# Optimization experiments

Hardware: AMD Instinct MI355X
Metric: run time of the kernel (lower is better)

## Reference

```python
import jax, jax.numpy as jnp
import numpy as np

B, N0, D0, N1, D1 = 128, 64, 32, 64, 32
K = 65  # depthwise conv kernel size
SCALE = 5.0
FOCUS = 3.0
EPS_Z = float(jnp.finfo(jnp.float32).eps)


def setup_inputs() -> dict:
    key = jax.random.key(0)
    k1, k2, k3, kw, kc, kb = jax.random.split(key, 6)
    x1 = jax.random.normal(k1, (B, N0, D0), dtype=jnp.float32)
    x2 = jax.random.normal(k2, (B, N0, D0), dtype=jnp.float32)
    x3 = jax.random.normal(k3, (B, N0, D0), dtype=jnp.float32)
    # kaiming_normal_ on W [N1, N0, D0, D1]: fan_in = N0*D0*D1 per torch default on 4D
    fan_in = N0 * D0 * D1
    W = jax.random.normal(kw, (N1, N0, D0, D1), dtype=jnp.float32) * np.sqrt(2.0 / fan_in)
    # Conv1d(N1*D1, N1*D1, K, groups=N1): weight [out_ch, in_ch/groups, K]
    cin_g = D1
    bound = 1.0 / np.sqrt(cin_g * K)
    conv_w = jax.random.uniform(kc, (N1 * D1, cin_g, K), dtype=jnp.float32, minval=-bound, maxval=bound)
    conv_b = jax.random.uniform(kb, (N1 * D1,), dtype=jnp.float32, minval=-bound, maxval=bound)
    return {"x1": x1, "x2": x2, "x3": x3, "W": W, "conv_w": conv_w, "conv_b": conv_b}


def _transform(x, W):
    # x: [B, N0, D0], W: [N1, N0, D0, D1] -> u: [B, N1*D1, N0]
    u = jnp.einsum('bji,kjiz->bkjz', x, W)        # [B, N1, N0, D1]
    u = jnp.transpose(u, (0, 1, 3, 2))             # [B, N1, D1, N0]
    return u.reshape(u.shape[0], N1 * D1, N0)


def _focus(u):
    # ReLU kernel + focusing-factor renormalization along last dim
    u = jax.nn.relu(u) + 1e-6
    u = u / SCALE
    n = jnp.linalg.norm(u, axis=-1, keepdims=True)
    up = u ** FOCUS
    return up / jnp.linalg.norm(up, axis=-1, keepdims=True) * n


def _squash(x, eps=1e-20):
    norm = jnp.linalg.norm(x, axis=-1, keepdims=True)
    coef = 1.0 - 1.0 / (jnp.exp(norm) + eps)
    return coef * (x / (norm + eps))


def reference(x1, x2, x3, W, conv_w, conv_b):
    u1 = _focus(_transform(x1, W))  # [B, N1*D1, N0]
    u2 = _focus(_transform(x2, W))
    u3 = _focus(_transform(x3, W))
    z = 1.0 / (jnp.einsum('bic,bc->bi', u1, u1.sum(axis=1)) + EPS_Z)  # [B, N1*D1]
    kv = jnp.einsum('bjc,bjd->bcd', u2, u3)                           # [B, N0, N0]
    x = jnp.einsum('bic,bcd,bi->bid', u1, kv, z)                      # [B, N1*D1, N0]
    # grouped (depthwise-per-capsule) conv1d, 'same' padding
    y = jax.lax.conv_general_dilated(
        x, conv_w, window_strides=(1,), padding=[(K // 2, K // 2)],
        dimension_numbers=('NCH', 'OIH', 'NCH'), feature_group_count=N1)
    y = y + conv_b[None, :, None]
    out = (x + y).sum(axis=-1).reshape(-1, N1, D1)  # [B, N1, D1]
    return _squash(out)
```

## Files before the change

kernel.cpp:

```cpp
#include <hip/hip_runtime.h>
#include <cstddef>

#define NB 128
#define NT 64
#define ND 32
#define NG 64
#define NC 2048
#define KW 65
#define EPSZ 1.1920928955078125e-07f

#define OFF_URAW 0ull
#define SZ_URAW  (3ull * NB * NT * NC)
#define OFF_F    (OFF_URAW + SZ_URAW)
#define SZ_F     (3ull * NB * NC)
#define OFF_S1   (OFF_F + SZ_F)
#define SZ_S1    ((unsigned long long)NB * NT)
#define OFF_KV   (OFF_S1 + SZ_S1)
#define SZ_KV    ((unsigned long long)NB * NT * NT)

__global__ __launch_bounds__(256) void k_transform(
    const float* __restrict__ x1, const float* __restrict__ x2,
    const float* __restrict__ x3, const float* __restrict__ W,
    float* __restrict__ uraw) {
  int bid = blockIdx.x;
  int j   = bid & 63;
  int nt  = (bid >> 6) & 15;
  int inp = bid >> 10;
  const float* x = (inp == 0) ? x1 : ((inp == 1) ? x2 : x3);
  float* uout = uraw + (size_t)inp * ((size_t)NB * NT * NC);

  __shared__ float as[32][132];
  __shared__ float bs[32][132];
  int tid = threadIdx.x;

  {
    int b = tid >> 1, h = tid & 1;
    const float* xp = x + ((size_t)b * NT + j) * ND + h * 16;
#pragma unroll
    for (int q = 0; q < 4; ++q) {
      float4 v = *reinterpret_cast<const float4*>(xp + q * 4);
      int i0 = h * 16 + q * 4;
      as[i0 + 0][b] = v.x; as[i0 + 1][b] = v.y;
      as[i0 + 2][b] = v.z; as[i0 + 3][b] = v.w;
    }
  }
  {
    int kk = tid >> 6, u = tid & 63;
    int i = u >> 1, h = u & 1;
    const float* wp = W + (((size_t)(nt * 4 + kk) * NT + j) * ND + i) * ND + h * 16;
#pragma unroll
    for (int q = 0; q < 4; ++q) {
      float4 v = *reinterpret_cast<const float4*>(wp + q * 4);
      int c0 = kk * 32 + h * 16 + q * 4;
      bs[i][c0 + 0] = v.x; bs[i][c0 + 1] = v.y;
      bs[i][c0 + 2] = v.z; bs[i][c0 + 3] = v.w;
    }
  }
  __syncthreads();

  int tm = tid & 15, tn = tid >> 4;
  int m0 = tm * 8, n0 = tn * 8;
  float acc[8][8];
#pragma unroll
  for (int a = 0; a < 8; ++a)
#pragma unroll
    for (int c = 0; c < 8; ++c) acc[a][c] = 0.f;

#pragma unroll 4
  for (int kk = 0; kk < 32; ++kk) {
    float4 a0 = *reinterpret_cast<const float4*>(&as[kk][m0]);
    float4 a1 = *reinterpret_cast<const float4*>(&as[kk][m0 + 4]);
    float4 b0 = *reinterpret_cast<const float4*>(&bs[kk][n0]);
    float4 b1 = *reinterpret_cast<const float4*>(&bs[kk][n0 + 4]);
    float av[8] = {a0.x, a0.y, a0.z, a0.w, a1.x, a1.y, a1.z, a1.w};
    float bv[8] = {b0.x, b0.y, b0.z, b0.w, b1.x, b1.y, b1.z, b1.w};
#pragma unroll
    for (int mi = 0; mi < 8; ++mi)
#pragma unroll
      for (int ni = 0; ni < 8; ++ni)
        acc[mi][ni] = fmaf(av[mi], bv[ni], acc[mi][ni]);
  }

#pragma unroll
  for (int mi = 0; mi < 8; ++mi) {
    float* cp = uout + ((size_t)(m0 + mi) * NT + j) * NC + nt * 128 + n0;
    float4 v0 = {acc[mi][0], acc[mi][1], acc[mi][2], acc[mi][3]};
    float4 v1 = {acc[mi][4], acc[mi][5], acc[mi][6], acc[mi][7]};
    *reinterpret_cast<float4*>(cp)     = v0;
    *reinterpret_cast<float4*>(cp + 4) = v1;
  }
}

__global__ __launch_bounds__(256) void k_factors(
    const float* __restrict__ uraw, float* __restrict__ f) {
  int bid = blockIdx.x;
  const float* u = uraw + (size_t)bid * ((size_t)NT * NC);
  int tid = threadIdx.x;
  float s2[8], s6[8];
#pragma unroll
  for (int q = 0; q < 8; ++q) { s2[q] = 0.f; s6[q] = 0.f; }
  for (int t = 0; t < NT; ++t) {
    const float* row = u + (size_t)t * NC;
#pragma unroll
    for (int q = 0; q < 8; ++q) {
      float v = row[tid + q * 256];
      float up = (fmaxf(v, 0.f) + 1e-6f) * 0.2f;
      float p2 = up * up;
      float p3 = p2 * up;
      s2[q] += p2;
      s6[q] += p3 * p3;
    }
  }
#pragma unroll
  for (int q = 0; q < 8; ++q)
    f[(size_t)bid * NC + tid + q * 256] = sqrtf(s2[q]) / sqrtf(s6[q]);
}

__global__ void k_zero(float* __restrict__ p, int n) {
  int i = blockIdx.x * blockDim.x + threadIdx.x;
  int stride = gridDim.x * blockDim.x;
  for (; i < n; i += stride) p[i] = 0.f;
}

__global__ __launch_bounds__(256) void k_kv_s1(
    const float* __restrict__ uraw, const float* __restrict__ f,
    float* __restrict__ kv, float* __restrict__ s1) {
  int b = blockIdx.x >> 2, chq = blockIdx.x & 3;
  int chbase = chq * 512;
  const float* u1 = uraw + (size_t)b * ((size_t)NT * NC);
  const float* u2 = u1 + (size_t)NB * NT * NC;
  const float* u3 = u2 + (size_t)NB * NT * NC;
  const float* f1 = f + (size_t)b * NC;
  const float* f2 = f1 + (size_t)NB * NC;
  const float* f3 = f2 + (size_t)NB * NC;

  __shared__ float a2[64][68];
  __shared__ float a3[64][68];
  __shared__ float red[64][4];
  int tid = threadIdx.x;

  {
    int t = tid >> 2, cq = tid & 3;
    const float* up = u1 + (size_t)t * NC + chbase + cq * 128;
    const float* fp = f1 + chbase + cq * 128;
    float acc = 0.f;
#pragma unroll 4
    for (int q = 0; q < 32; ++q) {
      float4 v  = *reinterpret_cast<const float4*>(up + q * 4);
      float4 fv = *reinterpret_cast<const float4*>(fp + q * 4);
      float vv[4] = {v.x, v.y, v.z, v.w};
      float ff[4] = {fv.x, fv.y, fv.z, fv.w};
#pragma unroll
      for (int r = 0; r < 4; ++r) {
        float uu = (fmaxf(vv[r], 0.f) + 1e-6f) * 0.2f;
        acc += uu * uu * uu * ff[r];
      }
    }
    red[t][cq] = acc;
  }
  __syncthreads();
  if (tid < 64)
    atomicAdd(&s1[b * NT + tid],
              red[tid][0] + red[tid][1] + red[tid][2] + red[tid][3]);

  int tm = tid & 15, tn = tid >> 4;
  float acc[4][4];
#pragma unroll
  for (int r = 0; r < 4; ++r)
#pragma unroll
    for (int q = 0; q < 4; ++q) acc[r][q] = 0.f;

  for (int tile = 0; tile < 8; ++tile) {
    int ch0 = chbase + tile * 64;
    __syncthreads();
    {
      int t = tid >> 2, c4 = tid & 3;
#pragma unroll
      for (int q = 0; q < 4; ++q) {
        int c = c4 * 16 + q * 4;
        float4 v2 = *reinterpret_cast<const float4*>(u2 + (size_t)t * NC + ch0 + c);
        float4 g2 = *reinterpret_cast<const float4*>(f2 + ch0 + c);
        float4 v3 = *reinterpret_cast<const float4*>(u3 + (size_t)t * NC + ch0 + c);
        float4 g3 = *reinterpret_cast<const float4*>(f3 + ch0 + c);
        float vv2[4] = {v2.x, v2.y, v2.z, v2.w};
        float gg2[4] = {g2.x, g2.y, g2.z, g2.w};
        float vv3[4] = {v3.x, v3.y, v3.z, v3.w};
        float gg3[4] = {g3.x, g3.y, g3.z, g3.w};
#pragma unroll
        for (int r = 0; r < 4; ++r) {
          float uu = (fmaxf(vv2[r], 0.f) + 1e-6f) * 0.2f;
          a2[c + r][t] = uu * uu * uu * gg2[r];
          float ww = (fmaxf(vv3[r], 0.f) + 1e-6f) * 0.2f;
          a3[c + r][t] = ww * ww * ww * gg3[r];
        }
      }
    }
    __syncthreads();
#pragma unroll 8
    for (int ch = 0; ch < 64; ++ch) {
      float4 av = *reinterpret_cast<const float4*>(&a2[ch][tm * 4]);
      float4 bv = *reinterpret_cast<const float4*>(&a3[ch][tn * 4]);
      float aa[4] = {av.x, av.y, av.z, av.w};
      float bb[4] = {bv.x, bv.y, bv.z, bv.w};
#pragma unroll
      for (int r = 0; r < 4; ++r)
#pragma unroll
        for (int q = 0; q < 4; ++q)
          acc[r][q] = fmaf(aa[r], bb[q], acc[r][q]);
    }
  }
#pragma unroll
  for (int r = 0; r < 4; ++r)
#pragma unroll
    for (int q = 0; q < 4; ++q)
      atomicAdd(&kv[(size_t)b * (NT * NT) + (tm * 4 + r) * NT + tn * 4 + q],
                acc[r][q]);
}

__global__ __launch_bounds__(64) void k_cwt(
    const float* __restrict__ cw, float* __restrict__ cwt) {
  int o = blockIdx.x;
  int tid = threadIdx.x;
  __shared__ float row[32 * KW];
  for (int i = tid; i < 32 * KW; i += 64) row[i] = cw[(size_t)o * (32 * KW) + i];
  __syncthreads();
  int jj = tid, j = jj + 1;
  for (int ci = 0; ci < 32; ++ci) {
    float v = 0.f;
    if (j <= 32) v -= row[ci * KW + j + 32];
    if (j >= 32 && j <= 63) v += row[ci * KW + j - 32];
    if (j == 64) {
      float s = 0.f;
      for (int k = 32; k <= 64; ++k) s += row[ci * KW + k];
      v += s;
    }
    cwt[(size_t)o * 2048 + ci * 64 + jj] = v;
  }
}

__global__ __launch_bounds__(256) void k_pre(
    const float* __restrict__ uraw, const float* __restrict__ f,
    const float* __restrict__ kvg, const float* __restrict__ s1g,
    float* __restrict__ pre) {
  int b = blockIdx.x >> 2, q = blockIdx.x & 3;
  int chbase = q * 512;
  const float* u1 = uraw + (size_t)b * ((size_t)NT * NC);
  const float* f1 = f + (size_t)b * NC;
  int tid = threadIdx.x;

  __shared__ float kvpreL[64][68];
  __shared__ float s1L[64];
  __shared__ float utL[64][132];

#pragma unroll
  for (int qq = 0; qq < 16; ++qq) {
    int i = tid + qq * 256;
    kvpreL[i >> 6][i & 63] = kvg[(size_t)b * (NT * NT) + i];
  }
  if (tid < 64) s1L[tid] = s1g[b * NT + tid];
  __syncthreads();
  if (tid < 64) {
    float run = 0.f;
    for (int t2 = 0; t2 < 64; ++t2) {
      run += kvpreL[tid][t2];
      kvpreL[tid][t2] = run;
    }
  }

  int cg = tid >> 3, tg = tid & 7;
  for (int tile = 0; tile < 4; ++tile) {
    int ch0 = chbase + tile * 128;
    __syncthreads();
    {
      int t = tid >> 2, c4 = tid & 3;
      const float* up = u1 + (size_t)t * NC + ch0 + c4 * 32;
      const float* fp = f1 + ch0 + c4 * 32;
#pragma unroll
      for (int qq = 0; qq < 8; ++qq) {
        float4 v  = *reinterpret_cast<const float4*>(up + qq * 4);
        float4 fv = *reinterpret_cast<const float4*>(fp + qq * 4);
        float vv[4] = {v.x, v.y, v.z, v.w};
        float ff[4] = {fv.x, fv.y, fv.z, fv.w};
#pragma unroll
        for (int r = 0; r < 4; ++r) {
          float uu = (fmaxf(vv[r], 0.f) + 1e-6f) * 0.2f;
          utL[t][c4 * 33 + qq * 4 + r] = uu * uu * uu * ff[r];
        }
      }
    }
    __syncthreads();

    int cl = cg * 4;
    int sk = (cl >> 5) * 33 + (cl & 31);
    float acc[4][8];
#pragma unroll
    for (int r = 0; r < 4; ++r)
#pragma unroll
      for (int c = 0; c < 8; ++c) acc[r][c] = 0.f;
    float accz[4] = {0.f, 0.f, 0.f, 0.f};

#pragma unroll 4
    for (int t1 = 0; t1 < 64; ++t1) {
      float4 a = *reinterpret_cast<const float4*>(&utL[t1][sk]);
      float s = s1L[t1];
      float4 k0 = *reinterpret_cast<const float4*>(&kvpreL[t1][tg * 8]);
      float4 k1 = *reinterpret_cast<const float4*>(&kvpreL[t1][tg * 8 + 4]);
      float aa[4] = {a.x, a.y, a.z, a.w};
      float kk[8] = {k0.x, k0.y, k0.z, k0.w, k1.x, k1.y, k1.z, k1.w};
#pragma unroll
      for (int r = 0; r < 4; ++r) {
        accz[r] = fmaf(aa[r], s, accz[r]);
#pragma unroll
        for (int c = 0; c < 8; ++c)
          acc[r][c] = fmaf(aa[r], kk[c], acc[r][c]);
      }
    }
#pragma unroll
    for (int r = 0; r < 4; ++r) {
      float z = 1.f / (accz[r] + EPSZ);
      float* pp = pre + ((size_t)b * NC + ch0 + cl + r) * 64 + tg * 8;
      float4 o0 = {acc[r][0] * z, acc[r][1] * z, acc[r][2] * z, acc[r][3] * z};
      float4 o1 = {acc[r][4] * z, acc[r][5] * z, acc[r][6] * z, acc[r][7] * z};
      *reinterpret_cast<float4*>(pp)     = o0;
      *reinterpret_cast<float4*>(pp + 4) = o1;
    }
  }
}

__global__ __launch_bounds__(256) void k_gemm(
    const float* __restrict__ pre, const float* __restrict__ cwt,
    const float* __restrict__ cb, float* __restrict__ out) {
  int g = blockIdx.x >> 2, bq = blockIdx.x & 3;
  int b0 = bq * 32;
  int tid = threadIdx.x;
  int oh = tid & 15, bh = tid >> 4;

  __shared__ float preL[32][68];
  __shared__ float cwtL[32][68];

  float a00 = 0.f, a01 = 0.f, a10 = 0.f, a11 = 0.f;
  float xs00 = 0.f, xs01 = 0.f, xs10 = 0.f, xs11 = 0.f;

  for (int kc = 0; kc < 32; ++kc) {
    __syncthreads();
    {
      int r8 = tid >> 3, s8 = tid & 7;
      const float* ps = pre + ((size_t)(b0 + r8) * NC + g * 32) * 64 + kc * 64 + s8 * 8;
      float4 p0 = *reinterpret_cast<const float4*>(ps);
      float4 p1 = *reinterpret_cast<const float4*>(ps + 4);
      *reinterpret_cast<float4*>(&preL[r8][s8 * 8])     = p0;
      *reinterpret_cast<float4*>(&preL[r8][s8 * 8 + 4]) = p1;
      const float* cs = cwt + (size_t)(g * 32 + r8) * 2048 + kc * 64 + s8 * 8;
      float4 c0 = *reinterpret_cast<const float4*>(cs);
      float4 c1 = *reinterpret_cast<const float4*>(cs + 4);
      *reinterpret_cast<float4*>(&cwtL[r8][s8 * 8])     = c0;
      *reinterpret_cast<float4*>(&cwtL[r8][s8 * 8 + 4]) = c1;
    }
    __syncthreads();

    if (kc == oh)      { xs00 = preL[bh][63]; xs10 = preL[bh + 16][63]; }
    if (kc == oh + 16) { xs01 = preL[bh][63]; xs11 = preL[bh + 16][63]; }

#pragma unroll
    for (int kk = 0; kk < 64; kk += 4) {
      float4 p0 = *reinterpret_cast<const float4*>(&preL[bh][kk]);
      float4 p1 = *reinterpret_cast<const float4*>(&preL[bh + 16][kk]);
      float4 c0 = *reinterpret_cast<const float4*>(&cwtL[oh][kk]);
      float4 c1 = *reinterpret_cast<const float4*>(&cwtL[oh + 16][kk]);
      a00 = fmaf(p0.x, c0.x, a00); a00 = fmaf(p0.y, c0.y, a00);
      a00 = fmaf(p0.z, c0.z, a00); a00 = fmaf(p0.w, c0.w, a00);
      a01 = fmaf(p0.x, c1.x, a01); a01 = fmaf(p0.y, c1.y, a01);
      a01 = fmaf(p0.z, c1.z, a01); a01 = fmaf(p0.w, c1.w, a01);
      a10 = fmaf(p1.x, c0.x, a10); a10 = fmaf(p1.y, c0.y, a10);
      a10 = fmaf(p1.z, c0.z, a10); a10 = fmaf(p1.w, c0.w, a10);
      a11 = fmaf(p1.x, c1.x, a11); a11 = fmaf(p1.y, c1.y, a11);
      a11 = fmaf(p1.z, c1.z, a11); a11 = fmaf(p1.w, c1.w, a11);
    }
  }

  float cb0 = cb[g * 32 + oh], cb1 = cb[g * 32 + oh + 16];
  float v00 = a00 + xs00 + 64.f * cb0;
  float v01 = a01 + xs01 + 64.f * cb1;
  float v10 = a10 + xs10 + 64.f * cb0;
  float v11 = a11 + xs11 + 64.f * cb1;

  float sqA = v00 * v00 + v01 * v01;
  float sqB = v10 * v10 + v11 * v11;
#pragma unroll
  for (int m = 8; m >= 1; m >>= 1) {
    sqA += __shfl_xor(sqA, m, 16);
    sqB += __shfl_xor(sqB, m, 16);
  }
  float nA = sqrtf(sqA), nB = sqrtf(sqB);
  float cA = 1.f - 1.f / (expf(nA) + 1e-20f);
  float cB = 1.f - 1.f / (expf(nB) + 1e-20f);
  float iA = cA / (nA + 1e-20f), iB = cB / (nB + 1e-20f);

  size_t baseA = ((size_t)(b0 + bh) * NG + g) * ND;
  size_t baseB = ((size_t)(b0 + bh + 16) * NG + g) * ND;
  out[baseA + oh]      = v00 * iA;
  out[baseA + oh + 16] = v01 * iA;
  out[baseB + oh]      = v10 * iB;
  out[baseB + oh + 16] = v11 * iB;
}

extern "C" void kernel_launch(void* const* d_in, const int* in_sizes, int n_in,
                              void* d_out, int out_size, void* d_ws, size_t ws_size,
                              hipStream_t stream) {
  const float* x1 = (const float*)d_in[0];
  const float* x2 = (const float*)d_in[1];
  const float* x3 = (const float*)d_in[2];
  const float* W  = (const float*)d_in[3];
  const float* cw = (const float*)d_in[4];
  const float* cb = (const float*)d_in[5];
  float* out = (float*)d_out;

  float* ws   = (float*)d_ws;
  float* uraw = ws + OFF_URAW;
  float* f    = ws + OFF_F;
  float* s1   = ws + OFF_S1;
  float* kv   = ws + OFF_KV;
  float* pre  = uraw + (size_t)NB * NT * NC;
  float* cwt  = uraw + 2ull * NB * NT * NC;

  k_transform<<<3072, 256, 0, stream>>>(x1, x2, x3, W, uraw);
  k_factors<<<384, 256, 0, stream>>>(uraw, f);
  k_zero<<<512, 256, 0, stream>>>(s1, (int)(SZ_S1 + SZ_KV));
  k_kv_s1<<<512, 256, 0, stream>>>(uraw, f, kv, s1);
  k_cwt<<<2048, 64, 0, stream>>>(cw, cwt);
  k_pre<<<512, 256, 0, stream>>>(uraw, f, kv, s1, pre);
  k_gemm<<<256, 256, 0, stream>>>(pre, cwt, cb, out);
}
```

Before: 361.6 us.

## Raise grid parallelism across factor, kv, pre and conv-GEMM kernels with split-K atomics

Splits k_factors into 1536 blocks, each covering a 512-channel quarter of one batch and input, and moves the s1 reduction into k_factors using wave shuffles and atomics. k_kv and k_pre now use 8 channel chunks per batch instead of 4. The final conv GEMM is rewritten as a split-K kernel that accumulates into a zeroed ysum buffer with atomics, followed by a separate k_out kernel that applies the squash. The goal is to fill more CUs on the small grids, at the cost of extra launches, extra atomics and u1 being read twice in k_factors.

```diff
diff --git a/kernel.cpp b/kernel.cpp
--- a/kernel.cpp
+++ b/kernel.cpp
@@ -92,28 +92,46 @@
 }
 
 __global__ __launch_bounds__(256) void k_factors(
-    const float* __restrict__ uraw, float* __restrict__ f) {
+    const float* __restrict__ uraw, float* __restrict__ f,
+    float* __restrict__ s1) {
   int bid = blockIdx.x;
-  const float* u = uraw + (size_t)bid * ((size_t)NT * NC);
-  int tid = threadIdx.x;
-  float s2[8], s6[8];
-#pragma unroll
-  for (int q = 0; q < 8; ++q) { s2[q] = 0.f; s6[q] = 0.f; }
+  int q = bid & 3, b = (bid >> 2) & 127, inp = bid >> 9;
+  const float* u = uraw + ((size_t)inp * NB + b) * ((size_t)NT * NC);
+  int tid = threadIdx.x;
+  int ch = q * 512 + tid * 2;
+
+  float s2a = 0.f, s6a = 0.f, s2b = 0.f, s6b = 0.f;
   for (int t = 0; t < NT; ++t) {
-    const float* row = u + (size_t)t * NC;
-#pragma unroll
-    for (int q = 0; q < 8; ++q) {
-      float v = row[tid + q * 256];
-      float up = (fmaxf(v, 0.f) + 1e-6f) * 0.2f;
-      float p2 = up * up;
-      float p3 = p2 * up;
-      s2[q] += p2;
-      s6[q] += p3 * p3;
-    }
-  }
-#pragma unroll
-  for (int q = 0; q < 8; ++q)
-    f[(size_t)bid * NC + tid + q * 256] = sqrtf(s2[q]) / sqrtf(s6[q]);
+    float2 v = *reinterpret_cast<const float2*>(u + (size_t)t * NC + ch);
+    float ua = (fmaxf(v.x, 0.f) + 1e-6f) * 0.2f;
+    float p2a = ua * ua, p3a = p2a * ua;
+    s2a += p2a; s6a += p3a * p3a;
+    float ub = (fmaxf(v.y, 0.f) + 1e-6f) * 0.2f;
+    float p2b = ub * ub, p3b = p2b * ub;
+    s2b += p2b; s6b += p3b * p3b;
+  }
+  float fa = sqrtf(s2a) / sqrtf(s6a);
+  float fb = sqrtf(s2b) / sqrtf(s6b);
+  float2 fv = {fa, fb};
+  *reinterpret_cast<float2*>(f + ((size_t)inp * NB + b) * NC + ch) = fv;
+
+  if (inp == 0) {
+    __shared__ float part[NT][4];
+    int wid = tid >> 6, lane = tid & 63;
+    for (int t = 0; t < NT; ++t) {
+      float2 v = *reinterpret_cast<const float2*>(u + (size_t)t * NC + ch);
+      float ua = (fmaxf(v.x, 0.f) + 1e-6f) * 0.2f;
+      float ub = (fmaxf(v.y, 0.f) + 1e-6f) * 0.2f;
+      float val = ua * ua * ua * fa + ub * ub * ub * fb;
+#pragma unroll
+      for (int m = 32; m >= 1; m >>= 1) val += __shfl_xor(val, m, 64);
+      if (lane == 0) part[t][wid] = val;
+    }
+    __syncthreads();
+    if (tid < NT)
+      atomicAdd(&s1[b * NT + tid],
+                part[tid][0] + part[tid][1] + part[tid][2] + part[tid][3]);
+  }
 }
 
 __global__ void k_zero(float* __restrict__ p, int n) {
@@ -122,46 +140,19 @@
   for (; i < n; i += stride) p[i] = 0.f;
 }
 
-__global__ __launch_bounds__(256) void k_kv_s1(
+__global__ __launch_bounds__(256) void k_kv(
     const float* __restrict__ uraw, const float* __restrict__ f,
-    float* __restrict__ kv, float* __restrict__ s1) {
-  int b = blockIdx.x >> 2, chq = blockIdx.x & 3;
-  int chbase = chq * 512;
-  const float* u1 = uraw + (size_t)b * ((size_t)NT * NC);
-  const float* u2 = u1 + (size_t)NB * NT * NC;
-  const float* u3 = u2 + (size_t)NB * NT * NC;
-  const float* f1 = f + (size_t)b * NC;
-  const float* f2 = f1 + (size_t)NB * NC;
-  const float* f3 = f2 + (size_t)NB * NC;
+    float* __restrict__ kv) {
+  int b = blockIdx.x >> 3, chq = blockIdx.x & 7;
+  int chbase = chq * 256;
+  const float* u2 = uraw + ((size_t)NB + b) * ((size_t)NT * NC);
+  const float* u3 = uraw + (2ull * NB + b) * ((size_t)NT * NC);
+  const float* f2 = f + ((size_t)NB + b) * NC;
+  const float* f3 = f + (2ull * NB + b) * NC;
 
   __shared__ float a2[64][68];
   __shared__ float a3[64][68];
-  __shared__ float red[64][4];
-  int tid = threadIdx.x;
-
-  {
-    int t = tid >> 2, cq = tid & 3;
-    const float* up = u1 + (size_t)t * NC + chbase + cq * 128;
-    const float* fp = f1 + chbase + cq * 128;
-    float acc = 0.f;
-#pragma unroll 4
-    for (int q = 0; q < 32; ++q) {
-      float4 v  = *reinterpret_cast<const float4*>(up + q * 4);
-      float4 fv = *reinterpret_cast<const float4*>(fp + q * 4);
-      float vv[4] = {v.x, v.y, v.z, v.w};
-      float ff[4] = {fv.x, fv.y, fv.z, fv.w};
-#pragma unroll
-      for (int r = 0; r < 4; ++r) {
-        float uu = (fmaxf(vv[r], 0.f) + 1e-6f) * 0.2f;
-        acc += uu * uu * uu * ff[r];
-      }
-    }
-    red[t][cq] = acc;
-  }
-  __syncthreads();
-  if (tid < 64)
-    atomicAdd(&s1[b * NT + tid],
-              red[tid][0] + red[tid][1] + red[tid][2] + red[tid][3]);
+  int tid = threadIdx.x;
 
   int tm = tid & 15, tn = tid >> 4;
   float acc[4][4];
@@ -170,7 +161,7 @@
 #pragma unroll
     for (int q = 0; q < 4; ++q) acc[r][q] = 0.f;
 
-  for (int tile = 0; tile < 8; ++tile) {
+  for (int tile = 0; tile < 4; ++tile) {
     int ch0 = chbase + tile * 64;
     __syncthreads();
     {
@@ -242,8 +233,8 @@
     const float* __restrict__ uraw, const float* __restrict__ f,
     const float* __restrict__ kvg, const float* __restrict__ s1g,
     float* __restrict__ pre) {
-  int b = blockIdx.x >> 2, q = blockIdx.x & 3;
-  int chbase = q * 512;
+  int b = blockIdx.x >> 3, q = blockIdx.x & 7;
+  int chbase = q * 256;
   const float* u1 = uraw + (size_t)b * ((size_t)NT * NC);
   const float* f1 = f + (size_t)b * NC;
   int tid = threadIdx.x;
@@ -268,7 +259,7 @@
   }
 
   int cg = tid >> 3, tg = tid & 7;
-  for (int tile = 0; tile < 4; ++tile) {
+  for (int tile = 0; tile < 2; ++tile) {
     int ch0 = chbase + tile * 128;
     __syncthreads();
     {
@@ -329,79 +320,85 @@
 
 __global__ __launch_bounds__(256) void k_gemm(
     const float* __restrict__ pre, const float* __restrict__ cwt,
+    float* __restrict__ ysum) {
+  int g = blockIdx.x >> 3, ks = blockIdx.x & 7;
+  int tid = threadIdx.x;
+  int oh = tid & 7, bh = tid >> 3;
+
+  __shared__ float AsT[64][132];
+  __shared__ float BsT[64][36];
+
+  float acc[4][4];
+#pragma unroll
+  for (int i = 0; i < 4; ++i)
+#pragma unroll
+    for (int j = 0; j < 4; ++j) acc[i][j] = 0.f;
+
+  for (int kc = 0; kc < 4; ++kc) {
+    int ci = ks * 4 + kc;
+    __syncthreads();
+    {
+      int bb = tid >> 1, jh = (tid & 1) * 32;
+      const float* ap = pre + ((size_t)bb * NC + g * 32 + ci) * 64 + jh;
+#pragma unroll
+      for (int qq = 0; qq < 8; ++qq) {
+        float4 v = *reinterpret_cast<const float4*>(ap + qq * 4);
+        int jj = jh + qq * 4;
+        AsT[jj + 0][bb] = v.x; AsT[jj + 1][bb] = v.y;
+        AsT[jj + 2][bb] = v.z; AsT[jj + 3][bb] = v.w;
+      }
+    }
+    if (tid < 128) {
+      int o = tid >> 2, jh = (tid & 3) * 16;
+      const float* bp = cwt + (size_t)(g * 32 + o) * 2048 + ci * 64 + jh;
+#pragma unroll
+      for (int qq = 0; qq < 4; ++qq) {
+        float4 v = *reinterpret_cast<const float4*>(bp + qq * 4);
+        int jj = jh + qq * 4;
+        BsT[jj + 0][o] = v.x; BsT[jj + 1][o] = v.y;
+        BsT[jj + 2][o] = v.z; BsT[jj + 3][o] = v.w;
+      }
+    }
+    __syncthreads();
+
+#pragma unroll 8
+    for (int jj = 0; jj < 64; ++jj) {
+      float4 a = *reinterpret_cast<const float4*>(&AsT[jj][bh * 4]);
+      float4 bv = *reinterpret_cast<const float4*>(&BsT[jj][oh * 4]);
+      float aa[4] = {a.x, a.y, a.z, a.w};
+      float bb[4] = {bv.x, bv.y, bv.z, bv.w};
+#pragma unroll
+      for (int i = 0; i < 4; ++i)
+#pragma unroll
+        for (int j = 0; j < 4; ++j)
+          acc[i][j] = fmaf(aa[i], bb[j], acc[i][j]);
+    }
+  }
+
+#pragma unroll
+  for (int i = 0; i < 4; ++i)
+#pragma unroll
+    for (int j = 0; j < 4; ++j)
+      atomicAdd(&ysum[(size_t)(bh * 4 + i) * NC + g * 32 + oh * 4 + j],
+                acc[i][j]);
+}
+
+__global__ __launch_bounds__(256) void k_out(
+    const float* __restrict__ pre, const float* __restrict__ ysum,
     const float* __restrict__ cb, float* __restrict__ out) {
-  int g = blockIdx.x >> 2, bq = blockIdx.x & 3;
-  int b0 = bq * 32;
-  int tid = threadIdx.x;
-  int oh = tid & 15, bh = tid >> 4;
-
-  __shared__ float preL[32][68];
-  __shared__ float cwtL[32][68];
-
-  float a00 = 0.f, a01 = 0.f, a10 = 0.f, a11 = 0.f;
-  float xs00 = 0.f, xs01 = 0.f, xs10 = 0.f, xs11 = 0.f;
-
-  for (int kc = 0; kc < 32; ++kc) {
-    __syncthreads();
-    {
-      int r8 = tid >> 3, s8 = tid & 7;
-      const float* ps = pre + ((size_t)(b0 + r8) * NC + g * 32) * 64 + kc * 64 + s8 * 8;
-      float4 p0 = *reinterpret_cast<const float4*>(ps);
-      float4 p1 = *reinterpret_cast<const float4*>(ps + 4);
-      *reinterpret_cast<float4*>(&preL[r8][s8 * 8])     = p0;
-      *reinterpret_cast<float4*>(&preL[r8][s8 * 8 + 4]) = p1;
-      const float* cs = cwt + (size_t)(g * 32 + r8) * 2048 + kc * 64 + s8 * 8;
-      float4 c0 = *reinterpret_cast<const float4*>(cs);
-      float4 c1 = *reinterpret_cast<const float4*>(cs + 4);
-      *reinterpret_cast<float4*>(&cwtL[r8][s8 * 8])     = c0;
-      *reinterpret_cast<float4*>(&cwtL[r8][s8 * 8 + 4]) = c1;
-    }
-    __syncthreads();
-
-    if (kc == oh)      { xs00 = preL[bh][63]; xs10 = preL[bh + 16][63]; }
-    if (kc == oh + 16) { xs01 = preL[bh][63]; xs11 = preL[bh + 16][63]; }
-
-#pragma unroll
-    for (int kk = 0; kk < 64; kk += 4) {
-      float4 p0 = *reinterpret_cast<const float4*>(&preL[bh][kk]);
-      float4 p1 = *reinterpret_cast<const float4*>(&preL[bh + 16][kk]);
-      float4 c0 = *reinterpret_cast<const float4*>(&cwtL[oh][kk]);
-      float4 c1 = *reinterpret_cast<const float4*>(&cwtL[oh + 16][kk]);
-      a00 = fmaf(p0.x, c0.x, a00); a00 = fmaf(p0.y, c0.y, a00);
-      a00 = fmaf(p0.z, c0.z, a00); a00 = fmaf(p0.w, c0.w, a00);
-      a01 = fmaf(p0.x, c1.x, a01); a01 = fmaf(p0.y, c1.y, a01);
-      a01 = fmaf(p0.z, c1.z, a01); a01 = fmaf(p0.w, c1.w, a01);
-      a10 = fmaf(p1.x, c0.x, a10); a10 = fmaf(p1.y, c0.y, a10);
-      a10 = fmaf(p1.z, c0.z, a10); a10 = fmaf(p1.w, c0.w, a10);
-      a11 = fmaf(p1.x, c1.x, a11); a11 = fmaf(p1.y, c1.y, a11);
-      a11 = fmaf(p1.z, c1.z, a11); a11 = fmaf(p1.w, c1.w, a11);
-    }
-  }
-
-  float cb0 = cb[g * 32 + oh], cb1 = cb[g * 32 + oh + 16];
-  float v00 = a00 + xs00 + 64.f * cb0;
-  float v01 = a01 + xs01 + 64.f * cb1;
-  float v10 = a10 + xs10 + 64.f * cb0;
-  float v11 = a11 + xs11 + 64.f * cb1;
-
-  float sqA = v00 * v00 + v01 * v01;
-  float sqB = v10 * v10 + v11 * v11;
-#pragma unroll
-  for (int m = 8; m >= 1; m >>= 1) {
-    sqA += __shfl_xor(sqA, m, 16);
-    sqB += __shfl_xor(sqB, m, 16);
-  }
-  float nA = sqrtf(sqA), nB = sqrtf(sqB);
-  float cA = 1.f - 1.f / (expf(nA) + 1e-20f);
-  float cB = 1.f - 1.f / (expf(nB) + 1e-20f);
-  float iA = cA / (nA + 1e-20f), iB = cB / (nB + 1e-20f);
-
-  size_t baseA = ((size_t)(b0 + bh) * NG + g) * ND;
-  size_t baseB = ((size_t)(b0 + bh + 16) * NG + g) * ND;
-  out[baseA + oh]      = v00 * iA;
-  out[baseA + oh + 16] = v01 * iA;
-  out[baseB + oh]      = v10 * iB;
-  out[baseB + oh + 16] = v11 * iB;
+  int tid = threadIdx.x;
+  int b = blockIdx.x >> 3;
+  int g = (blockIdx.x & 7) * 8 + (tid >> 5);
+  int o = tid & 31;
+  int go = g * 32 + o;
+  float xs = pre[((size_t)b * NC + go) * 64 + 63];
+  float val = ysum[(size_t)b * NC + go] + xs + 64.f * cb[go];
+  float sq = val * val;
+#pragma unroll
+  for (int m = 16; m >= 1; m >>= 1) sq += __shfl_xor(sq, m, 32);
+  float norm = sqrtf(sq);
+  float coef = 1.f - 1.f / (expf(norm) + 1e-20f);
+  out[((size_t)b * NG + g) * ND + o] = coef * val / (norm + 1e-20f);
 }
 
 extern "C" void kernel_launch(void* const* d_in, const int* in_sizes, int n_in,
@@ -422,12 +419,15 @@
   float* kv   = ws + OFF_KV;
   float* pre  = uraw + (size_t)NB * NT * NC;
   float* cwt  = uraw + 2ull * NB * NT * NC;
+  float* ysum = uraw;
 
   k_transform<<<3072, 256, 0, stream>>>(x1, x2, x3, W, uraw);
-  k_factors<<<384, 256, 0, stream>>>(uraw, f);
-  k_zero<<<512, 256, 0, stream>>>(s1, (int)(SZ_S1 + SZ_KV));
-  k_kv_s1<<<512, 256, 0, stream>>>(uraw, f, kv, s1);
+  k_zero<<<256, 256, 0, stream>>>(s1, (int)(SZ_S1 + SZ_KV));
+  k_factors<<<1536, 256, 0, stream>>>(uraw, f, s1);
+  k_kv<<<1024, 256, 0, stream>>>(uraw, f, kv);
   k_cwt<<<2048, 64, 0, stream>>>(cw, cwt);
-  k_pre<<<512, 256, 0, stream>>>(uraw, f, kv, s1, pre);
-  k_gemm<<<256, 256, 0, stream>>>(pre, cwt, cb, out);
-}
+  k_pre<<<1024, 256, 0, stream>>>(uraw, f, kv, s1, pre);
+  k_zero<<<256, 256, 0, stream>>>(ysum, (int)(NB * NC));
+  k_gemm<<<512, 256, 0, stream>>>(pre, cwt, ysum);
+  k_out<<<1024, 256, 0, stream>>>(pre, ysum, cb, out);
+}
```

Result: slower. 397.4 us (+9.9%).

## Fold s1 reduction into factors kernel, retile kv GEMM per wave, widen grids

Applied to the files above, without the earlier changes.

The factors kernel is split over more blocks, four per batch-input pair. For input 1 it also computes the s1 row sums with wave shuffles and atomics, so the kv kernel no longer re-reads u1 for that reduction. The kv kernel is restructured so each wave owns a channel slice with an 8x8 register tile and XOR-swizzled LDS, and the partial tiles are reduced in LDS before the atomics. k_pre gets twice as many blocks with half the channel range each, to raise parallelism. The cost is extra re-reads of u1 in the factors kernel and more atomic and reduction overhead.

```diff
diff --git a/kernel.cpp b/kernel.cpp
--- a/kernel.cpp
+++ b/kernel.cpp
@@ -17,6 +17,11 @@
 #define SZ_S1    ((unsigned long long)NB * NT)
 #define OFF_KV   (OFF_S1 + SZ_S1)
 #define SZ_KV    ((unsigned long long)NB * NT * NT)
+
+__device__ __forceinline__ float foc(float v, float fv) {
+  float u = (fmaxf(v, 0.f) + 1e-6f) * 0.2f;
+  return u * u * u * fv;
+}
 
 __global__ __launch_bounds__(256) void k_transform(
     const float* __restrict__ x1, const float* __restrict__ x2,
@@ -92,28 +97,46 @@
 }
 
 __global__ __launch_bounds__(256) void k_factors(
-    const float* __restrict__ uraw, float* __restrict__ f) {
+    const float* __restrict__ uraw, float* __restrict__ f,
+    float* __restrict__ s1) {
   int bid = blockIdx.x;
-  const float* u = uraw + (size_t)bid * ((size_t)NT * NC);
+  int q = bid & 3, b = (bid >> 2) & 127, inp = bid >> 9;
+  const float* u = uraw + ((size_t)inp * NB + b) * ((size_t)NT * NC);
   int tid = threadIdx.x;
-  float s2[8], s6[8];
-#pragma unroll
-  for (int q = 0; q < 8; ++q) { s2[q] = 0.f; s6[q] = 0.f; }
+  int ch = q * 512 + tid * 2;
+
+  float s2a = 0.f, s6a = 0.f, s2b = 0.f, s6b = 0.f;
   for (int t = 0; t < NT; ++t) {
-    const float* row = u + (size_t)t * NC;
-#pragma unroll
-    for (int q = 0; q < 8; ++q) {
-      float v = row[tid + q * 256];
-      float up = (fmaxf(v, 0.f) + 1e-6f) * 0.2f;
-      float p2 = up * up;
-      float p3 = p2 * up;
-      s2[q] += p2;
-      s6[q] += p3 * p3;
-    }
-  }
-#pragma unroll
-  for (int q = 0; q < 8; ++q)
-    f[(size_t)bid * NC + tid + q * 256] = sqrtf(s2[q]) / sqrtf(s6[q]);
+    float2 v = *reinterpret_cast<const float2*>(u + (size_t)t * NC + ch);
+    float ua = (fmaxf(v.x, 0.f) + 1e-6f) * 0.2f;
+    float p2a = ua * ua, p3a = p2a * ua;
+    s2a += p2a; s6a += p3a * p3a;
+    float ub = (fmaxf(v.y, 0.f) + 1e-6f) * 0.2f;
+    float p2b = ub * ub, p3b = p2b * ub;
+    s2b += p2b; s6b += p3b * p3b;
+  }
+  float fa = sqrtf(s2a) / sqrtf(s6a);
+  float fb = sqrtf(s2b) / sqrtf(s6b);
+  float2 fv = {fa, fb};
+  *reinterpret_cast<float2*>(f + ((size_t)inp * NB + b) * NC + ch) = fv;
+
+  if (inp == 0) {
+    __shared__ float part[NT][4];
+    int wid = tid >> 6, lane = tid & 63;
+    for (int t = 0; t < NT; ++t) {
+      float2 v = *reinterpret_cast<const float2*>(u + (size_t)t * NC + ch);
+      float ua = (fmaxf(v.x, 0.f) + 1e-6f) * 0.2f;
+      float ub = (fmaxf(v.y, 0.f) + 1e-6f) * 0.2f;
+      float val = ua * ua * ua * fa + ub * ub * ub * fb;
+#pragma unroll
+      for (int m = 32; m >= 1; m >>= 1) val += __shfl_xor(val, m, 64);
+      if (lane == 0) part[t][wid] = val;
+    }
+    __syncthreads();
+    if (tid < NT)
+      atomicAdd(&s1[b * NT + tid],
+                part[tid][0] + part[tid][1] + part[tid][2] + part[tid][3]);
+  }
 }
 
 __global__ void k_zero(float* __restrict__ p, int n) {
@@ -122,99 +145,88 @@
   for (; i < n; i += stride) p[i] = 0.f;
 }
 
-__global__ __launch_bounds__(256) void k_kv_s1(
+__global__ __launch_bounds__(256) void k_kv(
     const float* __restrict__ uraw, const float* __restrict__ f,
-    float* __restrict__ kv, float* __restrict__ s1) {
-  int b = blockIdx.x >> 2, chq = blockIdx.x & 3;
-  int chbase = chq * 512;
-  const float* u1 = uraw + (size_t)b * ((size_t)NT * NC);
-  const float* u2 = u1 + (size_t)NB * NT * NC;
-  const float* u3 = u2 + (size_t)NB * NT * NC;
-  const float* f1 = f + (size_t)b * NC;
-  const float* f2 = f1 + (size_t)NB * NC;
-  const float* f3 = f2 + (size_t)NB * NC;
-
-  __shared__ float a2[64][68];
-  __shared__ float a3[64][68];
-  __shared__ float red[64][4];
-  int tid = threadIdx.x;
-
-  {
-    int t = tid >> 2, cq = tid & 3;
-    const float* up = u1 + (size_t)t * NC + chbase + cq * 128;
-    const float* fp = f1 + chbase + cq * 128;
-    float acc = 0.f;
-#pragma unroll 4
-    for (int q = 0; q < 32; ++q) {
-      float4 v  = *reinterpret_cast<const float4*>(up + q * 4);
-      float4 fv = *reinterpret_cast<const float4*>(fp + q * 4);
-      float vv[4] = {v.x, v.y, v.z, v.w};
-      float ff[4] = {fv.x, fv.y, fv.z, fv.w};
-#pragma unroll
-      for (int r = 0; r < 4; ++r) {
-        float uu = (fmaxf(vv[r], 0.f) + 1e-6f) * 0.2f;
-        acc += uu * uu * uu * ff[r];
+    float* __restrict__ kv) {
+  int b = blockIdx.x >> 2, ks = blockIdx.x & 3;
+  int wv = threadIdx.x >> 6, lane = threadIdx.x & 63;
+  const float* u2 = uraw + ((size_t)NB + b) * ((size_t)NT * NC);
+  const float* u3 = uraw + (2ull * NB + b) * ((size_t)NT * NC);
+  const float* f2 = f + ((size_t)NB + b) * NC;
+  const float* f3 = f + (2ull * NB + b) * NC;
+
+  __shared__ float ldsF[16384];
+  float* L2 = ldsF + wv * 4096;
+  float* L3 = L2 + 2048;
+
+  int tm = lane >> 3, tn = lane & 7;
+  int sr = lane >> 3, c4 = lane & 7;
+
+  float acc[8][8];
+#pragma unroll
+  for (int i = 0; i < 8; ++i)
+#pragma unroll
+    for (int j = 0; j < 8; ++j) acc[i][j] = 0.f;
+
+  for (int chunk = 0; chunk < 4; ++chunk) {
+    int ch0 = ks * 512 + wv * 128 + chunk * 32;
+    float4 f2q = *reinterpret_cast<const float4*>(f2 + ch0 + c4 * 4);
+    float4 f3q = *reinterpret_cast<const float4*>(f3 + ch0 + c4 * 4);
+#pragma unroll
+    for (int it = 0; it < 8; ++it) {
+      int t = it * 8 + sr;
+      int q4s = c4 ^ sr ^ it;
+      float4 v2 = *reinterpret_cast<const float4*>(u2 + (size_t)t * NC + ch0 + c4 * 4);
+      float4 v3 = *reinterpret_cast<const float4*>(u3 + (size_t)t * NC + ch0 + c4 * 4);
+      float4 w2 = {foc(v2.x, f2q.x), foc(v2.y, f2q.y), foc(v2.z, f2q.z), foc(v2.w, f2q.w)};
+      float4 w3 = {foc(v3.x, f3q.x), foc(v3.y, f3q.y), foc(v3.z, f3q.z), foc(v3.w, f3q.w)};
+      *reinterpret_cast<float4*>(L2 + t * 32 + q4s * 4) = w2;
+      *reinterpret_cast<float4*>(L3 + t * 32 + q4s * 4) = w3;
+    }
+
+#pragma unroll
+    for (int kp = 0; kp < 16; ++kp) {
+      int q4 = kp >> 1, h = (kp & 1) * 2;
+      float2 af[8], bf[8];
+#pragma unroll
+      for (int i = 0; i < 8; ++i)
+        af[i] = *reinterpret_cast<const float2*>(
+            L2 + (tm * 8 + i) * 32 + ((q4 ^ i ^ tm) * 4 + h));
+#pragma unroll
+      for (int j = 0; j < 8; ++j)
+        bf[j] = *reinterpret_cast<const float2*>(
+            L3 + (tn * 8 + j) * 32 + ((q4 ^ j ^ tn) * 4 + h));
+#pragma unroll
+      for (int i = 0; i < 8; ++i)
+#pragma unroll
+        for (int j = 0; j < 8; ++j)
+          acc[i][j] = fmaf(af[i].y, bf[j].y, fmaf(af[i].x, bf[j].x, acc[i][j]));
+    }
+  }
+
+  __syncthreads();
+  if (wv > 0) {
+    float* dp = ldsF + (wv - 1) * 4224 + lane * 66;
+#pragma unroll
+    for (int i = 0; i < 8; ++i)
+#pragma unroll
+      for (int j = 0; j < 8; ++j) dp[i * 8 + j] = acc[i][j];
+  }
+  __syncthreads();
+  if (wv == 0) {
+    float* kvp = kv + (size_t)b * (NT * NT);
+    const float* d0 = ldsF + lane * 66;
+    const float* d1 = ldsF + 4224 + lane * 66;
+    const float* d2 = ldsF + 8448 + lane * 66;
+#pragma unroll
+    for (int i = 0; i < 8; ++i)
+#pragma unroll
+      for (int j = 0; j < 8; ++j) {
+        int c = i * 8 + j;
+        atomicAdd(&kvp[(tm * 8 + i) * 64 + tn * 8 + j],
+                  acc[i][j] + d0[c] + d1[c] + d2[c]);
       }
-    }
-    red[t][cq] = acc;
-  }
-  __syncthreads();
-  if (tid < 64)
-    atomicAdd(&s1[b * NT + tid],
-              red[tid][0] + red[tid][1] + red[tid][2] + red[tid][3]);
-
-  int tm = tid & 15, tn = tid >> 4;
-  float acc[4][4];
-#pragma unroll
-  for (int r = 0; r < 4; ++r)
-#pragma unroll
-    for (int q = 0; q < 4; ++q) acc[r][q] = 0.f;
-
-  for (int tile = 0; tile < 8; ++tile) {
-    int ch0 = chbase + tile * 64;
-    __syncthreads();
-    {
-      int t = tid >> 2, c4 = tid & 3;
-#pragma unroll
-      for (int q = 0; q < 4; ++q) {
-        int c = c4 * 16 + q * 4;
-        float4 v2 = *reinterpret_cast<const float4*>(u2 + (size_t)t * NC + ch0 + c);
-        float4 g2 = *reinterpret_cast<const float4*>(f2 + ch0 + c);
-        float4 v3 = *reinterpret_cast<const float4*>(u3 + (size_t)t * NC + ch0 + c);
-        float4 g3 = *reinterpret_cast<const float4*>(f3 + ch0 + c);
-        float vv2[4] = {v2.x, v2.y, v2.z, v2.w};
-        float gg2[4] = {g2.x, g2.y, g2.z, g2.w};
-        float vv3[4] = {v3.x, v3.y, v3.z, v3.w};
-        float gg3[4] = {g3.x, g3.y, g3.z, g3.w};
-#pragma unroll
-        for (int r = 0; r < 4; ++r) {
-          float uu = (fmaxf(vv2[r], 0.f) + 1e-6f) * 0.2f;
-          a2[c + r][t] = uu * uu * uu * gg2[r];
-          float ww = (fmaxf(vv3[r], 0.f) + 1e-6f) * 0.2f;
-          a3[c + r][t] = ww * ww * ww * gg3[r];
-        }
-      }
-    }
-    __syncthreads();
-#pragma unroll 8
-    for (int ch = 0; ch < 64; ++ch) {
-      float4 av = *reinterpret_cast<const float4*>(&a2[ch][tm * 4]);
-      float4 bv = *reinterpret_cast<const float4*>(&a3[ch][tn * 4]);
-      float aa[4] = {av.x, av.y, av.z, av.w};
-      float bb[4] = {bv.x, bv.y, bv.z, bv.w};
-#pragma unroll
-      for (int r = 0; r < 4; ++r)
-#pragma unroll
-        for (int q = 0; q < 4; ++q)
-          acc[r][q] = fmaf(aa[r], bb[q], acc[r][q]);
-    }
-  }
-#pragma unroll
-  for (int r = 0; r < 4; ++r)
-#pragma unroll
-    for (int q = 0; q < 4; ++q)
-      atomicAdd(&kv[(size_t)b * (NT * NT) + (tm * 4 + r) * NT + tn * 4 + q],
-                acc[r][q]);
+  }
 }
 
 __global__ __launch_bounds__(64) void k_cwt(
@@ -242,8 +254,8 @@
     const float* __restrict__ uraw, const float* __restrict__ f,
     const float* __restrict__ kvg, const float* __restrict__ s1g,
     float* __restrict__ pre) {
-  int b = blockIdx.x >> 2, q = blockIdx.x & 3;
-  int chbase = q * 512;
+  int b = blockIdx.x >> 3, q = blockIdx.x & 7;
+  int chbase = q * 256;
   const float* u1 = uraw + (size_t)b * ((size_t)NT * NC);
   const float* f1 = f + (size_t)b * NC;
   int tid = threadIdx.x;
@@ -268,7 +280,7 @@
   }
 
   int cg = tid >> 3, tg = tid & 7;
-  for (int tile = 0; tile < 4; ++tile) {
+  for (int tile = 0; tile < 2; ++tile) {
     int ch0 = chbase + tile * 128;
     __syncthreads();
     {
@@ -424,10 +436,10 @@
   float* cwt  = uraw + 2ull * NB * NT * NC;
 
   k_transform<<<3072, 256, 0, stream>>>(x1, x2, x3, W, uraw);
-  k_factors<<<384, 256, 0, stream>>>(uraw, f);
-  k_zero<<<512, 256, 0, stream>>>(s1, (int)(SZ_S1 + SZ_KV));
-  k_kv_s1<<<512, 256, 0, stream>>>(uraw, f, kv, s1);
+  k_zero<<<256, 256, 0, stream>>>(s1, (int)(SZ_S1 + SZ_KV));
+  k_factors<<<1536, 256, 0, stream>>>(uraw, f, s1);
+  k_kv<<<512, 256, 0, stream>>>(uraw, f, kv);
   k_cwt<<<2048, 64, 0, stream>>>(cw, cwt);
-  k_pre<<<512, 256, 0, stream>>>(uraw, f, kv, s1, pre);
+  k_pre<<<1024, 256, 0, stream>>>(uraw, f, kv, s1, pre);
   k_gemm<<<256, 256, 0, stream>>>(pre, cwt, cb, out);
 }
```

New measurement: 422.9 us. 1.17x slower.
